# Kernel optimization log

Hardware: AMD Instinct MI355X
Metric: run time of the kernel (lower is better)

The kernel has to match this reference:

```python
import jax, jax.numpy as jnp
import numpy as np

N_NODES = 100000
N_EDGES = 1600000
IN_DIM = 256
HID0 = 128
HID1 = 64


def _glorot(key, shape):
    fan_in, fan_out = shape[0], shape[1]
    lim = (6.0 / (fan_in + fan_out)) ** 0.5
    return jax.random.uniform(key, shape, jnp.float32, -lim, lim)


def setup_inputs() -> dict:
    key = jax.random.key(0)
    ks = jax.random.split(key, 8)
    x = jax.random.normal(ks[0], (N_NODES, IN_DIM), jnp.float32)
    edge_index = jax.random.randint(ks[1], (2, N_EDGES), 0, N_NODES, jnp.int32)
    return {
        "x": x,
        "edge_index": edge_index,
        "W_conv": _glorot(ks[2], (IN_DIM, HID0)),
        "b_conv": jnp.zeros((HID0,), jnp.float32),
        "W_lin": _glorot(ks[3], (HID0, HID1)),
        "b_lin": jnp.zeros((HID1,), jnp.float32),
        "W_dec1": _glorot(ks[4], (HID1, HID0)),
        "b_dec1": jnp.zeros((HID0,), jnp.float32),
        "W_dec2": _glorot(ks[5], (HID0, IN_DIM)),
        "b_dec2": jnp.zeros((IN_DIM,), jnp.float32),
    }


def gcn_conv(x, edge_index, W, b):
    # PyG GCNConv: add self-loops, symmetric normalization, linear (no bias), scatter-add, + bias
    n = x.shape[0]
    loop = jnp.arange(n, dtype=edge_index.dtype)
    row = jnp.concatenate([edge_index[0], loop])  # source nodes
    col = jnp.concatenate([edge_index[1], loop])  # destination nodes
    deg = jax.ops.segment_sum(jnp.ones_like(col, jnp.float32), col, num_segments=n)
    dis = jnp.where(deg > 0, jax.lax.rsqrt(jnp.maximum(deg, 1e-12)), 0.0)
    norm = dis[row] * dis[col]  # [E+N]
    h = x @ W  # [N, hid]
    msg = h[row] * norm[:, None]  # gather over edges
    out = jax.ops.segment_sum(msg, col, num_segments=n)  # scatter-add
    return out + b


def reference(x, edge_index, W_conv, b_conv, W_lin, b_lin, W_dec1, b_dec1, W_dec2, b_dec2):
    # Encoder
    h = gcn_conv(x, edge_index, W_conv, b_conv)
    h = jax.nn.relu(h)
    z = h @ W_lin + b_lin
    # Decoder
    d = jax.nn.relu(z @ W_dec1 + b_dec1)
    out = d @ W_dec2 + b_dec2
    return out
```

## Files before the change

### kernel.cpp

```cpp
#include <hip/hip_runtime.h>
#include <hip/hip_bf16.h>


#define N_DIM 256
#define H0 128
#define H1 64
#define CHUNK 8192

typedef __bf16 bf16x8 __attribute__((ext_vector_type(8)));
typedef short  short8 __attribute__((ext_vector_type(8)));
typedef short  s16x4  __attribute__((ext_vector_type(4)));
typedef float  f32x16 __attribute__((ext_vector_type(16)));
typedef unsigned short ushort_t;

__device__ inline unsigned bf_hi(float v) {
    unsigned b = __float_as_uint(v);
    return (b + 0x7FFF + ((b >> 16) & 1)) >> 16;
}
__device__ inline float bf_f(unsigned bits) { return __uint_as_float(bits << 16); }

__global__ __launch_bounds__(256) void prep(
    const float* __restrict__ Wc, const float* __restrict__ Wl,
    const float* __restrict__ Wd1, const float* __restrict__ Wd2,
    ushort_t* __restrict__ wc, ushort_t* __restrict__ wl,
    ushort_t* __restrict__ wd1, ushort_t* __restrict__ wd2,
    int* __restrict__ tot, int nbk) {
    const int S1 = 256 * 128, S2 = S1 + 128 * 64, S3 = S2 + 64 * 128, S4 = S3 + 128 * 256;
    int idx = blockIdx.x * 256 + threadIdx.x;
    const float* W; ushort_t* hi; int K, N, loc, planeSz;
    if (idx < S1)      { W = Wc;  hi = wc;  K = 256; N = 128; loc = idx;      planeSz = S1; }
    else if (idx < S2) { W = Wl;  hi = wl;  K = 128; N = 64;  loc = idx - S1; planeSz = 128 * 64; }
    else if (idx < S3) { W = Wd1; hi = wd1; K = 64;  N = 128; loc = idx - S2; planeSz = 64 * 128; }
    else if (idx < S4) { W = Wd2; hi = wd2; K = 128; N = 256; loc = idx - S3; planeSz = 128 * 256; }
    else {
        int i = idx - S4;
        if (i < nbk) tot[i] = 0;
        return;
    }
    int n = loc / K, k = loc - n * K;
    float v = W[(size_t)k * N + n];
    unsigned h = bf_hi(v);
    hi[loc] = (ushort_t)h;
    hi[planeSz + loc] = (ushort_t)bf_hi(v - bf_f(h));
}

__global__ __launch_bounds__(256) void bucket_hist(const int* __restrict__ dst,
                                                   int* __restrict__ tot, int E, int nbk) {
    __shared__ int h[512];
    h[threadIdx.x] = 0; h[threadIdx.x + 256] = 0;
    __syncthreads();
    int stride = gridDim.x * 256;
    for (int e = blockIdx.x * 256 + threadIdx.x; e < E; e += stride)
        atomicAdd(&h[dst[e] >> 8], 1);
    __syncthreads();
    #pragma unroll
    for (int q = 0; q < 2; ++q) {
        int b = threadIdx.x + q * 256;
        if (b < nbk && h[b]) atomicAdd(&tot[b], h[b]);
    }
}

__global__ __launch_bounds__(256) void bucket_scan(const int* __restrict__ tot,
                                                   int* __restrict__ bbase,
                                                   int* __restrict__ bcur,
                                                   int* __restrict__ row_ptr,
                                                   int nbk, int Nn, int E) {
    __shared__ int sA[512], sB[512];
    int t = threadIdx.x;
    int v0 = (t < nbk) ? tot[t] : 0;
    int v1 = (t + 256 < nbk) ? tot[t + 256] : 0;
    sA[t] = v0; sA[t + 256] = v1;
    __syncthreads();
    int *a = sA, *b = sB;
    for (int off = 1; off < 512; off <<= 1) {
        b[t]       = a[t]       + (t >= off ? a[t - off] : 0);
        b[t + 256] = a[t + 256] + (t + 256 >= off ? a[t + 256 - off] : 0);
        __syncthreads();
        int* w = a; a = b; b = w;
    }
    if (t < nbk)       { bbase[t] = a[t] - v0;             bcur[t] = a[t] - v0; }
    if (t + 256 < nbk) { bbase[t + 256] = a[t + 256] - v1; bcur[t + 256] = a[t + 256] - v1; }
    if (t == 0) { bbase[nbk] = E; row_ptr[Nn] = E; }
}

__global__ __launch_bounds__(256) void bucket_scatter(
    const int* __restrict__ src, const int* __restrict__ dst,
    int* __restrict__ bcur, int* __restrict__ tmp, int E, int nbk) {
    __shared__ int pk[CHUNK];
    __shared__ ushort_t bk[CHUNK];
    __shared__ int hcnt[512], wcur[512];
    int base = blockIdx.x * CHUNK;
    int cnt = min(CHUNK, E - base);
    hcnt[threadIdx.x] = 0; hcnt[threadIdx.x + 256] = 0;
    __syncthreads();
    for (int i = threadIdx.x; i < cnt; i += 256) {
        int s = src[base + i], d = dst[base + i];
        int b = d >> 8;
        pk[i] = (s << 8) | (d & 255);
        bk[i] = (ushort_t)b;
        atomicAdd(&hcnt[b], 1);
    }
    __syncthreads();
    #pragma unroll
    for (int q = 0; q < 2; ++q) {
        int b = threadIdx.x + q * 256;
        if (b < nbk) {
            int c = hcnt[b];
            wcur[b] = c ? atomicAdd(&bcur[b], c) : 0;
        }
    }
    __syncthreads();
    for (int i = threadIdx.x; i < cnt; i += 256) {
        int b = bk[i];
        int p = atomicAdd(&wcur[b], 1);
        tmp[p] = pk[i];
    }
}

__global__ __launch_bounds__(256) void fine_csr(const int* __restrict__ bbase,
                                                const int* __restrict__ tmp,
                                                int* __restrict__ csr,
                                                int* __restrict__ row_ptr, int Nn) {
    __shared__ int fcnt[256], sA[256], sB[256], fcur[256];
    int b = blockIdx.x;
    int rb = bbase[b], re = bbase[b + 1];
    int t = threadIdx.x;
    fcnt[t] = 0;
    __syncthreads();
    for (int i = rb + t; i < re; i += 256)
        atomicAdd(&fcnt[tmp[i] & 255], 1);
    __syncthreads();
    sA[t] = fcnt[t];
    __syncthreads();
    int *a = sA, *bb = sB;
    for (int off = 1; off < 256; off <<= 1) {
        bb[t] = a[t] + (t >= off ? a[t - off] : 0);
        __syncthreads();
        int* w = a; a = bb; bb = w;
    }
    int ex = a[t] - fcnt[t];
    fcur[t] = ex;
    int node = (b << 8) + t;
    if (node < Nn) row_ptr[node] = rb + ex;
    __syncthreads();
    for (int i = rb + t; i < re; i += 256) {
        int pkv = tmp[i];
        int p = atomicAdd(&fcur[pkv & 255], 1);
        csr[rb + p] = (unsigned)pkv >> 8;
    }
}

__global__ __launch_bounds__(256) void calc_dis(const int* __restrict__ row_ptr,
                                                float* __restrict__ dis, int Nn) {
    int i = blockIdx.x * 256 + threadIdx.x;
    if (i < Nn) dis[i] = rsqrtf((float)(row_ptr[i + 1] - row_ptr[i]) + 1.0f);
}

__global__ __launch_bounds__(256) void gather_nodes(
    const int* __restrict__ row_ptr, const int* __restrict__ csr,
    const float* __restrict__ dis, const ushort_t* __restrict__ hb,
    const float* __restrict__ b_conv, ushort_t* __restrict__ ra, int n) {
    int gid  = (blockIdx.x * 256 + threadIdx.x) >> 5;
    int lane = threadIdx.x & 31;
    if (gid >= n) return;
    const size_t loOff = (size_t)n * H0;
    int beg = row_ptr[gid], end = row_ptr[gid + 1];
    float dc = dis[gid];
    const int lo4 = lane * 4;
    ushort4 sh = *(const ushort4*)&hb[(size_t)gid * H0 + lo4];
    ushort4 sl = *(const ushort4*)&hb[loOff + (size_t)gid * H0 + lo4];
    float sx = bf_f(sh.x) + bf_f(sl.x);
    float sy = bf_f(sh.y) + bf_f(sl.y);
    float sz = bf_f(sh.z) + bf_f(sl.z);
    float sw = bf_f(sh.w) + bf_f(sl.w);
    int j = beg;
    for (; j + 2 <= end; j += 2) {
        int r0 = csr[j], r1 = csr[j + 1];
        ushort4 v0 = *(const ushort4*)&hb[(size_t)r0 * H0 + lo4];
        ushort4 v1 = *(const ushort4*)&hb[(size_t)r1 * H0 + lo4];
        sx += bf_f(v0.x) + bf_f(v1.x);
        sy += bf_f(v0.y) + bf_f(v1.y);
        sz += bf_f(v0.z) + bf_f(v1.z);
        sw += bf_f(v0.w) + bf_f(v1.w);
    }
    if (j < end) {
        int r0 = csr[j];
        ushort4 v0 = *(const ushort4*)&hb[(size_t)r0 * H0 + lo4];
        sx += bf_f(v0.x); sy += bf_f(v0.y); sz += bf_f(v0.z); sw += bf_f(v0.w);
    }
    float4 bv = *(const float4*)&b_conv[lo4];
    float ax = fmaxf(fmaf(sx, dc, bv.x), 0.f);
    float ay = fmaxf(fmaf(sy, dc, bv.y), 0.f);
    float az = fmaxf(fmaf(sz, dc, bv.z), 0.f);
    float aw = fmaxf(fmaf(sw, dc, bv.w), 0.f);
    ushort4 h4, l4;
    unsigned t;
    t = bf_hi(ax); h4.x = t; l4.x = (ushort_t)bf_hi(ax - bf_f(t));
    t = bf_hi(ay); h4.y = t; l4.y = (ushort_t)bf_hi(ay - bf_f(t));
    t = bf_hi(az); h4.z = t; l4.z = (ushort_t)bf_hi(az - bf_f(t));
    t = bf_hi(aw); h4.w = t; l4.w = (ushort_t)bf_hi(aw - bf_f(t));
    *(ushort4*)&ra[(size_t)gid * H0 + lo4] = h4;
    *(ushort4*)&ra[loOff + (size_t)gid * H0 + lo4] = l4;
}

template <int BM, int BN, int BK, int A_SPLIT, int BIAS, int RELU_O, int OUT_SPLIT, int OUT_SCALE>
__global__ __launch_bounds__(256, 5) void gemm_mfma(
    const float* __restrict__ A, const ushort_t* __restrict__ Asp,
    const ushort_t* __restrict__ Bt, const float* __restrict__ bias,
    const float* __restrict__ scale_m,
    float* __restrict__ C, ushort_t* __restrict__ Cs, int M, int K, int Nc) {
    constexpr int WN  = BN / 2;
    constexpr int FM  = BM / 64;
    constexpr int FNv = WN / 32;
    constexpr int LSA = 40;

    __shared__ short Ah[BM * LSA], Al[BM * LSA];
    __shared__ short Bh[BN * LSA], Bl[BN * LSA];

    const int tid  = threadIdx.x;
    const int lane = tid & 63, wid = tid >> 6;
    const int wm = wid >> 1, wn = wid & 1;
    const int l31 = lane & 31, l5 = lane >> 5;
    const int bm = blockIdx.x * BM;
    const int bn = blockIdx.y * BN;
    const size_t aLo = (size_t)M * K;
    const size_t bLo = (size_t)Nc * K;

    f32x16 acc[FM][FNv] = {};

    for (int k0 = 0; k0 < K; k0 += BK) {
        if (A_SPLIT) {
            #pragma unroll
            for (int it = 0; it < (BM * 4) / 256; ++it) {
                int u = it * 256 + tid;
                int m = u >> 2, kc = u & 3;
                int gm = bm + m;
                short8 h8 = {}, l8 = {};
                if (gm < M) {
                    size_t g = (size_t)gm * K + k0 + kc * 8;
                    h8 = *(const short8*)&Asp[g];
                    l8 = *(const short8*)&Asp[aLo + g];
                }
                *(short8*)&Ah[m * LSA + kc * 8] = h8;
                *(short8*)&Al[m * LSA + kc * 8] = l8;
            }
        } else {
            #pragma unroll
            for (int it = 0; it < (BM * BK) / (4 * 256); ++it) {
                int u = it * 256 + tid;
                int r = u >> 3, c4 = u & 7;
                int gr = bm + r;
                float4 v = make_float4(0.f, 0.f, 0.f, 0.f);
                if (gr < M) v = *(const float4*)&A[(size_t)gr * K + k0 + c4 * 4];
                s16x4 hi4, lo4;
                float f[4] = {v.x, v.y, v.z, v.w};
                #pragma unroll
                for (int i = 0; i < 4; ++i) {
                    unsigned hb_ = bf_hi(f[i]);
                    hi4[i] = (short)hb_;
                    lo4[i] = (short)bf_hi(f[i] - bf_f(hb_));
                }
                *(s16x4*)&Ah[r * LSA + c4 * 4] = hi4;
                *(s16x4*)&Al[r * LSA + c4 * 4] = lo4;
            }
        }
        #pragma unroll
        for (int it = 0; it < (BN * 4) / 256; ++it) {
            int u = it * 256 + tid;
            int nn = u >> 2, kc = u & 3;
            size_t g = (size_t)(bn + nn) * K + k0 + kc * 8;
            *(short8*)&Bh[nn * LSA + kc * 8] = *(const short8*)&Bt[g];
            *(short8*)&Bl[nn * LSA + kc * 8] = *(const short8*)&Bt[bLo + g];
        }
        __syncthreads();
        #pragma unroll
        for (int kh = 0; kh < 2; ++kh) {
            const int kcol = kh * 16 + l5 * 8;
            bf16x8 ah[FM], al[FM], bh[FNv], bl[FNv];
            #pragma unroll
            for (int fm = 0; fm < FM; ++fm) {
                int row = wm * (BM / 2) + fm * 32 + l31;
                ah[fm] = __builtin_bit_cast(bf16x8, *(const short8*)&Ah[row * LSA + kcol]);
                al[fm] = __builtin_bit_cast(bf16x8, *(const short8*)&Al[row * LSA + kcol]);
            }
            #pragma unroll
            for (int fn = 0; fn < FNv; ++fn) {
                int col = wn * WN + fn * 32 + l31;
                bh[fn] = __builtin_bit_cast(bf16x8, *(const short8*)&Bh[col * LSA + kcol]);
                bl[fn] = __builtin_bit_cast(bf16x8, *(const short8*)&Bl[col * LSA + kcol]);
            }
            #pragma unroll
            for (int fm = 0; fm < FM; ++fm)
                #pragma unroll
                for (int fn = 0; fn < FNv; ++fn) {
                    acc[fm][fn] = __builtin_amdgcn_mfma_f32_32x32x16_bf16(
                        al[fm], bh[fn], acc[fm][fn], 0, 0, 0);
                    acc[fm][fn] = __builtin_amdgcn_mfma_f32_32x32x16_bf16(
                        ah[fm], bl[fn], acc[fm][fn], 0, 0, 0);
                    acc[fm][fn] = __builtin_amdgcn_mfma_f32_32x32x16_bf16(
                        ah[fm], bh[fn], acc[fm][fn], 0, 0, 0);
                }
        }
        __syncthreads();
    }
    const size_t loOff = (size_t)M * Nc;
    int   ncols[FNv];
    float bvv[FNv];
    #pragma unroll
    for (int fn = 0; fn < FNv; ++fn) {
        ncols[fn] = bn + wn * WN + fn * 32 + l31;
        bvv[fn] = BIAS ? bias[ncols[fn]] : 0.f;
    }
    #pragma unroll
    for (int fm = 0; fm < FM; ++fm)
        #pragma unroll
        for (int j = 0; j < 16; ++j) {
            int gm = bm + wm * (BM / 2) + fm * 32 + (j & 3) + 8 * (j >> 2) + 4 * l5;
            if (gm >= M) continue;
            float sc = OUT_SCALE ? scale_m[gm] : 1.0f;
            #pragma unroll
            for (int fn = 0; fn < FNv; ++fn) {
                float v = fmaf(acc[fm][fn][j], sc, bvv[fn]);
                if (RELU_O) v = fmaxf(v, 0.f);
                if (OUT_SPLIT) {
                    unsigned hb_ = bf_hi(v);
                    Cs[(size_t)gm * Nc + ncols[fn]] = (ushort_t)hb_;
                    Cs[loOff + (size_t)gm * Nc + ncols[fn]] = (ushort_t)bf_hi(v - bf_f(hb_));
                } else {
                    C[(size_t)gm * Nc + ncols[fn]] = v;
                }
            }
        }
}

extern "C" void kernel_launch(void* const* d_in, const int* in_sizes, int n_in,
                              void* d_out, int out_size, void* d_ws, size_t ws_size,
                              hipStream_t stream) {
    const float* x      = (const float*)d_in[0];
    const int*   edge   = (const int*)d_in[1];
    const float* W_conv = (const float*)d_in[2];
    const float* b_conv = (const float*)d_in[3];
    const float* W_lin  = (const float*)d_in[4];
    const float* b_lin  = (const float*)d_in[5];
    const float* W_dec1 = (const float*)d_in[6];
    const float* b_dec1 = (const float*)d_in[7];
    const float* W_dec2 = (const float*)d_in[8];
    const float* b_dec2 = (const float*)d_in[9];
    float* out = (float*)d_out;

    const int Nn = in_sizes[0] / N_DIM;
    const int E  = in_sizes[1] / 2;
    const int* src = edge;
    const int* dst = edge + E;
    const int nbk = (Nn + 255) >> 8;

    ushort_t* wc_t  = (ushort_t*)d_ws;
    ushort_t* wl_t  = wc_t  + 2 * 256 * 128;
    ushort_t* wd1_t = wl_t  + 2 * 128 * 64;
    ushort_t* wd2_t = wd1_t + 2 * 64 * 128;
    ushort_t* hsl   = wd2_t + 2 * 128 * 256;
    ushort_t* rasl  = hsl + (size_t)2 * Nn * H0;
    int*   tmp      = (int*)(rasl + (size_t)2 * Nn * H0);
    int*   csr      = tmp + E;
    int*   tot      = csr + E;
    int*   bbase    = tot + nbk;
    int*   bcur     = bbase + nbk + 1;
    int*   row_ptr  = bcur + nbk;
    float* dis      = (float*)(row_ptr + Nn + 1);

    const int gM = (Nn + 63) / 64;

    const int prepTot = 256 * 128 + 128 * 64 + 64 * 128 + 128 * 256 + nbk;
    prep<<<(prepTot + 255) / 256, 256, 0, stream>>>(
        W_conv, W_lin, W_dec1, W_dec2, wc_t, wl_t, wd1_t, wd2_t, tot, nbk);
    bucket_hist<<<512, 256, 0, stream>>>(dst, tot, E, nbk);
    bucket_scan<<<1, 256, 0, stream>>>(tot, bbase, bcur, row_ptr, nbk, Nn, E);
    bucket_scatter<<<(E + CHUNK - 1) / CHUNK, 256, 0, stream>>>(src, dst, bcur, tmp, E, nbk);
    fine_csr<<<nbk, 256, 0, stream>>>(bbase, tmp, csr, row_ptr, Nn);
    calc_dis<<<(Nn + 255) / 256, 256, 0, stream>>>(row_ptr, dis, Nn);
    gemm_mfma<64, 128, 32, 0, 0, 0, 1, 1><<<dim3(gM, 1), 256, 0, stream>>>(
        x, nullptr, wc_t, nullptr, dis, nullptr, hsl, Nn, N_DIM, H0);
    gather_nodes<<<((size_t)Nn * 32 + 255) / 256, 256, 0, stream>>>(
        row_ptr, csr, dis, hsl, b_conv, rasl, Nn);
    gemm_mfma<64, 64, 32, 1, 1, 0, 1, 0><<<dim3(gM, 1), 256, 0, stream>>>(
        nullptr, rasl, wl_t, b_lin, nullptr, nullptr, hsl, Nn, H0, H1);
    gemm_mfma<64, 128, 32, 1, 1, 1, 1, 0><<<dim3(gM, 1), 256, 0, stream>>>(
        nullptr, hsl, wd1_t, b_dec1, nullptr, nullptr, rasl, Nn, H1, H0);
    gemm_mfma<64, 128, 32, 1, 1, 0, 0, 0><<<dim3(gM, 2), 256, 0, stream>>>(
        nullptr, rasl, wd2_t, b_dec2, nullptr, out, nullptr, Nn, H0, N_DIM);
}
```

Measured before the change: 436.1 us.

## Prefetch next GEMM K-tile into registers and fold degree calc into CSR build

The GEMM main loop now issues the global loads for the next K tile into registers before computing on the current shared-memory tile, then stores them after the MMA step. This overlaps global memory latency with MFMA work. Separately, the inverse-sqrt degree is computed inside fine_csr from the per-node counts, which removes the calc_dis kernel launch and its row_ptr reread. Prefetch registers increase register pressure, which may reduce occupancy under the 5-wave launch bound.

```diff
diff --git a/kernel.cpp b/kernel.cpp
--- a/kernel.cpp
+++ b/kernel.cpp
@@ -120,7 +120,8 @@
 __global__ __launch_bounds__(256) void fine_csr(const int* __restrict__ bbase,
                                                 const int* __restrict__ tmp,
                                                 int* __restrict__ csr,
-                                                int* __restrict__ row_ptr, int Nn) {
+                                                int* __restrict__ row_ptr,
+                                                float* __restrict__ dis, int Nn) {
     __shared__ int fcnt[256], sA[256], sB[256], fcur[256];
     int b = blockIdx.x;
     int rb = bbase[b], re = bbase[b + 1];
@@ -141,19 +142,16 @@
     int ex = a[t] - fcnt[t];
     fcur[t] = ex;
     int node = (b << 8) + t;
-    if (node < Nn) row_ptr[node] = rb + ex;
+    if (node < Nn) {
+        row_ptr[node] = rb + ex;
+        dis[node] = rsqrtf((float)fcnt[t] + 1.0f);
+    }
     __syncthreads();
     for (int i = rb + t; i < re; i += 256) {
         int pkv = tmp[i];
         int p = atomicAdd(&fcur[pkv & 255], 1);
         csr[rb + p] = (unsigned)pkv >> 8;
     }
-}
-
-__global__ __launch_bounds__(256) void calc_dis(const int* __restrict__ row_ptr,
-                                                float* __restrict__ dis, int Nn) {
-    int i = blockIdx.x * 256 + threadIdx.x;
-    if (i < Nn) dis[i] = rsqrtf((float)(row_ptr[i + 1] - row_ptr[i]) + 1.0f);
 }
 
 __global__ __launch_bounds__(256) void gather_nodes(
@@ -213,6 +211,9 @@
     constexpr int FM  = BM / 64;
     constexpr int FNv = WN / 32;
     constexpr int LSA = 40;
+    constexpr int A_IT  = (BM * 4) / 256;
+    constexpr int A_ITF = (BM * BK) / (4 * 256);
+    constexpr int B_IT  = (BN * 4) / 256;
 
     __shared__ short Ah[BM * LSA], Al[BM * LSA];
     __shared__ short Bh[BN * LSA], Bl[BN * LSA];
@@ -226,34 +227,61 @@
     const size_t aLo = (size_t)M * K;
     const size_t bLo = (size_t)Nc * K;
 
-    f32x16 acc[FM][FNv] = {};
-
-    for (int k0 = 0; k0 < K; k0 += BK) {
+    short8 pAh[A_IT], pAl[A_IT];
+    float4 pAf[A_ITF];
+    short8 pBh[B_IT], pBl[B_IT];
+
+    auto LOADA = [&](int k0) {
         if (A_SPLIT) {
             #pragma unroll
-            for (int it = 0; it < (BM * 4) / 256; ++it) {
+            for (int it = 0; it < A_IT; ++it) {
                 int u = it * 256 + tid;
                 int m = u >> 2, kc = u & 3;
                 int gm = bm + m;
-                short8 h8 = {}, l8 = {};
+                pAh[it] = short8{}; pAl[it] = short8{};
                 if (gm < M) {
                     size_t g = (size_t)gm * K + k0 + kc * 8;
-                    h8 = *(const short8*)&Asp[g];
-                    l8 = *(const short8*)&Asp[aLo + g];
+                    pAh[it] = *(const short8*)&Asp[g];
+                    pAl[it] = *(const short8*)&Asp[aLo + g];
                 }
-                *(short8*)&Ah[m * LSA + kc * 8] = h8;
-                *(short8*)&Al[m * LSA + kc * 8] = l8;
             }
         } else {
             #pragma unroll
-            for (int it = 0; it < (BM * BK) / (4 * 256); ++it) {
+            for (int it = 0; it < A_ITF; ++it) {
                 int u = it * 256 + tid;
                 int r = u >> 3, c4 = u & 7;
                 int gr = bm + r;
-                float4 v = make_float4(0.f, 0.f, 0.f, 0.f);
-                if (gr < M) v = *(const float4*)&A[(size_t)gr * K + k0 + c4 * 4];
+                pAf[it] = make_float4(0.f, 0.f, 0.f, 0.f);
+                if (gr < M) pAf[it] = *(const float4*)&A[(size_t)gr * K + k0 + c4 * 4];
+            }
+        }
+    };
+    auto LOADB = [&](int k0) {
+        #pragma unroll
+        for (int it = 0; it < B_IT; ++it) {
+            int u = it * 256 + tid;
+            int nn = u >> 2, kc = u & 3;
+            size_t g = (size_t)(bn + nn) * K + k0 + kc * 8;
+            pBh[it] = *(const short8*)&Bt[g];
+            pBl[it] = *(const short8*)&Bt[bLo + g];
+        }
+    };
+    auto STORE = [&]() {
+        if (A_SPLIT) {
+            #pragma unroll
+            for (int it = 0; it < A_IT; ++it) {
+                int u = it * 256 + tid;
+                int m = u >> 2, kc = u & 3;
+                *(short8*)&Ah[m * LSA + kc * 8] = pAh[it];
+                *(short8*)&Al[m * LSA + kc * 8] = pAl[it];
+            }
+        } else {
+            #pragma unroll
+            for (int it = 0; it < A_ITF; ++it) {
+                int u = it * 256 + tid;
+                int r = u >> 3, c4 = u & 7;
                 s16x4 hi4, lo4;
-                float f[4] = {v.x, v.y, v.z, v.w};
+                float f[4] = {pAf[it].x, pAf[it].y, pAf[it].z, pAf[it].w};
                 #pragma unroll
                 for (int i = 0; i < 4; ++i) {
                     unsigned hb_ = bf_hi(f[i]);
@@ -265,14 +293,22 @@
             }
         }
         #pragma unroll
-        for (int it = 0; it < (BN * 4) / 256; ++it) {
+        for (int it = 0; it < B_IT; ++it) {
             int u = it * 256 + tid;
             int nn = u >> 2, kc = u & 3;
-            size_t g = (size_t)(bn + nn) * K + k0 + kc * 8;
-            *(short8*)&Bh[nn * LSA + kc * 8] = *(const short8*)&Bt[g];
-            *(short8*)&Bl[nn * LSA + kc * 8] = *(const short8*)&Bt[bLo + g];
-        }
+            *(short8*)&Bh[nn * LSA + kc * 8] = pBh[it];
+            *(short8*)&Bl[nn * LSA + kc * 8] = pBl[it];
+        }
+    };
+
+    f32x16 acc[FM][FNv] = {};
+
+    LOADA(0); LOADB(0);
+    for (int k0 = 0; k0 < K; k0 += BK) {
+        STORE();
         __syncthreads();
+        int kn = k0 + BK;
+        if (kn < K) { LOADA(kn); LOADB(kn); }
         #pragma unroll
         for (int kh = 0; kh < 2; ++kh) {
             const int kcol = kh * 16 + l5 * 8;
@@ -376,8 +412,7 @@
     bucket_hist<<<512, 256, 0, stream>>>(dst, tot, E, nbk);
     bucket_scan<<<1, 256, 0, stream>>>(tot, bbase, bcur, row_ptr, nbk, Nn, E);
     bucket_scatter<<<(E + CHUNK - 1) / CHUNK, 256, 0, stream>>>(src, dst, bcur, tmp, E, nbk);
-    fine_csr<<<nbk, 256, 0, stream>>>(bbase, tmp, csr, row_ptr, Nn);
-    calc_dis<<<(Nn + 255) / 256, 256, 0, stream>>>(row_ptr, dis, Nn);
+    fine_csr<<<nbk, 256, 0, stream>>>(bbase, tmp, csr, row_ptr, dis, Nn);
     gemm_mfma<64, 128, 32, 0, 0, 0, 1, 1><<<dim3(gM, 1), 256, 0, stream>>>(
         x, nullptr, wc_t, nullptr, dis, nullptr, hsl, Nn, N_DIM, H0);
     gather_nodes<<<((size_t)Nn * 32 + 255) / 256, 256, 0, stream>>>(
```

Measured after the change: 429.1 us. About the same (-1.6%).
